# Kernel tuning notes

Hardware: AMD Instinct MI355X
Metric: run time of the kernel (lower is better)

## Reference

```python
import jax, jax.numpy as jnp
import numpy as np

MARGIN = 0.3
S = 15.0
LAMDA = 2.0

B, C = 8192, 10000


def setup_inputs() -> dict:
    key = jax.random.key(0)
    k1, k2 = jax.random.split(key)
    costh = jax.random.uniform(k1, (B, C), dtype=jnp.float32)  # cosine similarities
    label = jax.random.randint(k2, (B,), 0, C, dtype=jnp.int64)
    return {"costh": costh, "label": label}


def reference(costh, label):
    b = costh.shape[0]
    rows = jnp.arange(b)
    cos_t = costh[rows, label]                      # [B] target cosine
    delta = MARGIN * jnp.exp(1.0 - cos_t) / LAMDA   # [B] per-sample margin
    # subtract margin only at the target column, then scale
    logits = S * costh.at[rows, label].add(-delta)  # [B, C]
    logp = jax.nn.log_softmax(logits, axis=-1)
    loss = -jnp.mean(logp[rows, label])
    return loss
```

## Files before the change

### kernel.cpp

```cpp
#include <hip/hip_runtime.h>

#define MARGIN   0.3f
#define S_SCALE  15.0f
#define LAMDA    2.0f
#define NB       8192
#define NC       10000
#define MAXLOGIT 15.0f

__global__ __launch_bounds__(256) void dam_row_loss(const float* __restrict__ costh,
                                                    const int* __restrict__ label,
                                                    float* __restrict__ row_loss) {
    const int row = blockIdx.x;
    const int tid = threadIdx.x;
    const float* __restrict__ rowp = costh + (size_t)row * NC;

    float s = 0.0f;
    const float4* __restrict__ rp4 = (const float4*)rowp;
    const int n4 = NC / 4;
    for (int i = tid; i < n4; i += 256) {
        float4 v = rp4[i];
        s += __expf(fmaf(S_SCALE, v.x, -MAXLOGIT));
        s += __expf(fmaf(S_SCALE, v.y, -MAXLOGIT));
        s += __expf(fmaf(S_SCALE, v.z, -MAXLOGIT));
        s += __expf(fmaf(S_SCALE, v.w, -MAXLOGIT));
    }

    #pragma unroll
    for (int off = 32; off > 0; off >>= 1)
        s += __shfl_down(s, off, 64);
    __shared__ float wsum[4];
    if ((tid & 63) == 0) wsum[tid >> 6] = s;
    __syncthreads();

    if (tid == 0) {
        float tot = wsum[0] + wsum[1] + wsum[2] + wsum[3];
        const int lbl = label[row];
        const float cos_t = rowp[lbl];
        const float delta = (MARGIN / LAMDA) * __expf(1.0f - cos_t);
        const float t_logit = S_SCALE * (cos_t - delta);
        tot = tot - __expf(fmaf(S_SCALE, cos_t, -MAXLOGIT)) + __expf(t_logit - MAXLOGIT);
        const float lse = MAXLOGIT + __logf(tot);
        row_loss[row] = lse - t_logit;
    }
}

__global__ __launch_bounds__(256) void dam_reduce(const float* __restrict__ row_loss,
                                                  float* __restrict__ out) {
    const int tid = threadIdx.x;
    float s = 0.0f;
    for (int i = tid; i < NB; i += 256) s += row_loss[i];
    #pragma unroll
    for (int off = 32; off > 0; off >>= 1)
        s += __shfl_down(s, off, 64);
    __shared__ float wsum[4];
    if ((tid & 63) == 0) wsum[tid >> 6] = s;
    __syncthreads();
    if (tid == 0) out[0] = (wsum[0] + wsum[1] + wsum[2] + wsum[3]) * (1.0f / (float)NB);
}

extern "C" void kernel_launch(void* const* d_in, const int* in_sizes, int n_in,
                              void* d_out, int out_size, void* d_ws, size_t ws_size,
                              hipStream_t stream) {
    const float* costh = (const float*)d_in[0];
    const int*   label = (const int*)d_in[1];
    float* out = (float*)d_out;
    float* row_loss = (float*)d_ws;

    dam_row_loss<<<NB, 256, 0, stream>>>(costh, label, row_loss);
    dam_reduce<<<1, 256, 0, stream>>>(row_loss, out);
}
```

Before: 434.9 us.

## Fuse final reduction via atomicAdd and fully unroll row loads with exp2

Drops the separate reduction kernel: each block scales its row loss and atomically adds it into the output, which is zeroed by an async memset. The row loop is fully unrolled so all ten float4 loads per thread are issued up front, and exp is computed with the hardware exp2 using folded constants and four independent accumulators. This removes one kernel launch and a workspace round-trip and exposes more memory-level parallelism. The cost is 8192 atomics on a single address and a summation order that is no longer deterministic.

```diff
diff --git a/kernel.cpp b/kernel.cpp
--- a/kernel.cpp
+++ b/kernel.cpp
@@ -5,25 +5,33 @@
 #define LAMDA    2.0f
 #define NB       8192
 #define NC       10000
-#define MAXLOGIT 15.0f
+#define LOG2E    1.4426950408889634f
+#define K2       (S_SCALE * LOG2E)
+#define B2       (-S_SCALE * LOG2E)
 
 __global__ __launch_bounds__(256) void dam_row_loss(const float* __restrict__ costh,
                                                     const int* __restrict__ label,
-                                                    float* __restrict__ row_loss) {
+                                                    float* __restrict__ out) {
     const int row = blockIdx.x;
     const int tid = threadIdx.x;
     const float* __restrict__ rowp = costh + (size_t)row * NC;
+    const float4* __restrict__ rp4 = (const float4*)rowp;
 
-    float s = 0.0f;
-    const float4* __restrict__ rp4 = (const float4*)rowp;
-    const int n4 = NC / 4;
-    for (int i = tid; i < n4; i += 256) {
-        float4 v = rp4[i];
-        s += __expf(fmaf(S_SCALE, v.x, -MAXLOGIT));
-        s += __expf(fmaf(S_SCALE, v.y, -MAXLOGIT));
-        s += __expf(fmaf(S_SCALE, v.z, -MAXLOGIT));
-        s += __expf(fmaf(S_SCALE, v.w, -MAXLOGIT));
+    float4 v[10];
+    #pragma unroll
+    for (int j = 0; j < 9; ++j) v[j] = rp4[tid + 256 * j];
+    v[9] = make_float4(-INFINITY, -INFINITY, -INFINITY, -INFINITY);
+    if (tid < 196) v[9] = rp4[2304 + tid];
+
+    float s0 = 0.f, s1 = 0.f, s2 = 0.f, s3 = 0.f;
+    #pragma unroll
+    for (int j = 0; j < 10; ++j) {
+        s0 += __builtin_amdgcn_exp2f(fmaf(K2, v[j].x, B2));
+        s1 += __builtin_amdgcn_exp2f(fmaf(K2, v[j].y, B2));
+        s2 += __builtin_amdgcn_exp2f(fmaf(K2, v[j].z, B2));
+        s3 += __builtin_amdgcn_exp2f(fmaf(K2, v[j].w, B2));
     }
+    float s = (s0 + s1) + (s2 + s3);
 
     #pragma unroll
     for (int off = 32; off > 0; off >>= 1)
@@ -33,29 +41,16 @@
     __syncthreads();
 
     if (tid == 0) {
-        float tot = wsum[0] + wsum[1] + wsum[2] + wsum[3];
+        float tot = (wsum[0] + wsum[1]) + (wsum[2] + wsum[3]);
         const int lbl = label[row];
         const float cos_t = rowp[lbl];
         const float delta = (MARGIN / LAMDA) * __expf(1.0f - cos_t);
         const float t_logit = S_SCALE * (cos_t - delta);
-        tot = tot - __expf(fmaf(S_SCALE, cos_t, -MAXLOGIT)) + __expf(t_logit - MAXLOGIT);
-        const float lse = MAXLOGIT + __logf(tot);
-        row_loss[row] = lse - t_logit;
+        tot += __builtin_amdgcn_exp2f(fmaf(LOG2E, t_logit, B2))
+             - __builtin_amdgcn_exp2f(fmaf(K2, cos_t, B2));
+        const float lse = S_SCALE + __logf(tot);
+        atomicAdd(out, (lse - t_logit) * (1.0f / (float)NB));
     }
-}
-
-__global__ __launch_bounds__(256) void dam_reduce(const float* __restrict__ row_loss,
-                                                  float* __restrict__ out) {
-    const int tid = threadIdx.x;
-    float s = 0.0f;
-    for (int i = tid; i < NB; i += 256) s += row_loss[i];
-    #pragma unroll
-    for (int off = 32; off > 0; off >>= 1)
-        s += __shfl_down(s, off, 64);
-    __shared__ float wsum[4];
-    if ((tid & 63) == 0) wsum[tid >> 6] = s;
-    __syncthreads();
-    if (tid == 0) out[0] = (wsum[0] + wsum[1] + wsum[2] + wsum[3]) * (1.0f / (float)NB);
 }
 
 extern "C" void kernel_launch(void* const* d_in, const int* in_sizes, int n_in,
@@ -64,8 +59,7 @@
     const float* costh = (const float*)d_in[0];
     const int*   label = (const int*)d_in[1];
     float* out = (float*)d_out;
-    float* row_loss = (float*)d_ws;
 
-    dam_row_loss<<<NB, 256, 0, stream>>>(costh, label, row_loss);
-    dam_reduce<<<1, 256, 0, stream>>>(row_loss, out);
+    hipMemsetAsync(out, 0, sizeof(float), stream);
+    dam_row_loss<<<NB, 256, 0, stream>>>(costh, label, out);
 }
```

Result: no change. 439.5 us (+1.1%).
